# Kernel tuning notes

Hardware: AMD Instinct MI355X
Metric: run time of the kernel (lower is better)

## Reference

```python
import jax, jax.numpy as jnp
import numpy as np

NF = 10      # num RBF / Chebyshev features
GAMMA = 1.0
EMB = 10
H = 64
NHEADS = 2


def _rbf(d):
    centers = jnp.arange(1, NF + 1, dtype=d.dtype)
    return jnp.exp(-GAMMA * (centers - d[..., None]) ** 2)


def _cheb(a):
    feats = [jnp.ones_like(a), a]
    for _ in range(2, NF):
        feats.append(2 * a * feats[-1] - feats[-2])
    return jnp.stack(feats, -1)


def _gru_layer(xs, wih, whh, bih, bhh):
    # xs: [L, B, D] -> [L, B, H]; PyTorch gate order r, z, n
    B = xs.shape[1]
    def step(h, xt):
        gi = xt @ wih.T + bih
        gh = h @ whh.T + bhh
        ir, iz, inn = jnp.split(gi, 3, -1)
        hr, hz, hn = jnp.split(gh, 3, -1)
        r = jax.nn.sigmoid(ir + hr)
        z = jax.nn.sigmoid(iz + hz)
        n = jnp.tanh(inn + r * hn)
        hnew = (1 - z) * n + z * h
        return hnew, hnew
    h0 = jnp.zeros((B, H), xs.dtype)
    _, ys = jax.lax.scan(step, h0, xs)
    return ys


def _mha(x, in_w, in_b, out_w, out_b):
    B, L, E = x.shape
    hd = E // NHEADS
    qkv = x @ in_w.T + in_b
    q, k, v = jnp.split(qkv, 3, -1)
    sp = lambda t: t.reshape(B, L, NHEADS, hd).transpose(0, 2, 1, 3)
    q, k, v = sp(q), sp(k), sp(v)
    scale = 1.0 / float(np.sqrt(hd))
    att = jax.nn.softmax(jnp.einsum('bhqd,bhkd->bhqk', q, k) * scale, -1)
    o = jnp.einsum('bhqk,bhkd->bhqd', att, v).transpose(0, 2, 1, 3).reshape(B, L, E)
    return o @ out_w.T + out_b


def _ln(x, s, b):
    m = x.mean(-1, keepdims=True)
    v = ((x - m) ** 2).mean(-1, keepdims=True)
    return (x - m) / jnp.sqrt(v + 1e-5) * s + b


def setup_inputs() -> dict:
    key = jax.random.key(0)
    ks = jax.random.split(key, 48)
    N, L = 384, 256
    # bond rows: [atom_idx1, atom_idx2, bond_dist]; angle rows: [d1, d2, angle]
    idx1 = jax.random.randint(ks[0], (N, L), 1, 119).astype(jnp.float32)
    idx2 = jax.random.randint(ks[1], (N, L), 1, 119).astype(jnp.float32)
    dist = jax.random.uniform(ks[2], (N, L), minval=0.5, maxval=5.0)
    d1 = jax.random.uniform(ks[3], (N, L), minval=0.5, maxval=5.0)
    d2 = jax.random.uniform(ks[4], (N, L), minval=0.5, maxval=5.0)
    ang = jax.random.uniform(ks[5], (N, L), minval=-1.0, maxval=1.0)
    bond_x = jnp.stack([idx1, idx2, dist], 1)
    angle_x = jnp.stack([d1, d2, ang], 1)
    is_angle = (jnp.arange(N) % 3 == 2)
    x = jnp.where(is_angle[:, None, None], angle_x, bond_x)

    def nrm(k, shp, s=0.1):
        return jax.random.normal(k, shp) * s

    D_IN = 2 * EMB + NF  # 30
    inp = {
        'x': x,
        'emb': nrm(ks[6], (119, EMB), 1.0),
        'wih0': nrm(ks[7], (3 * H, D_IN)),
        'whh0': nrm(ks[8], (3 * H, H)),
        'bih0': nrm(ks[9], (3 * H,)),
        'bhh0': nrm(ks[10], (3 * H,)),
        'wih12': nrm(ks[11], (2, 3 * H, H)),
        'whh12': nrm(ks[12], (2, 3 * H, H)),
        'bih12': nrm(ks[13], (2, 3 * H)),
        'bhh12': nrm(ks[14], (2, 3 * H)),
        'in_w1': nrm(ks[15], (3 * H, H)),
        'in_b1': nrm(ks[16], (3 * H,)),
        'out_w1': nrm(ks[17], (H, H)),
        'out_b1': nrm(ks[18], (H,)),
        'in_w2': nrm(ks[19], (3 * H, H)),
        'in_b2': nrm(ks[20], (3 * H,)),
        'out_w2': nrm(ks[21], (H, H)),
        'out_b2': nrm(ks[22], (H,)),
        'ff_w1': nrm(ks[23], (1024, H)),
        'ff_b1': nrm(ks[24], (1024,)),
        'ff_w2': nrm(ks[25], (H, 1024)),
        'ff_b2': nrm(ks[26], (H,)),
        'ln1_s': jnp.ones((H,)), 'ln1_b': jnp.zeros((H,)),
        'ln2_s': jnp.ones((H,)), 'ln2_b': jnp.zeros((H,)),
        'ln3_s': jnp.ones((H,)), 'ln3_b': jnp.zeros((H,)),
        'ln4_s': jnp.ones((H,)), 'ln4_b': jnp.zeros((H,)),
        'fw1': nrm(ks[27], (256, H)), 'fb1': nrm(ks[28], (256,)),
        'fw2': nrm(ks[29], (64, 256)), 'fb2': nrm(ks[30], (64,)),
        'fw3': nrm(ks[31], (32, 64)), 'fb3': nrm(ks[32], (32,)),
        'fw4': nrm(ks[33], (1, 32)), 'fb4': nrm(ks[34], (1,)),
    }
    return inp


def reference(x, emb, wih0, whh0, bih0, bhh0, wih12, whh12, bih12, bhh12,
              in_w1, in_b1, out_w1, out_b1, in_w2, in_b2, out_w2, out_b2,
              ff_w1, ff_b1, ff_w2, ff_b2,
              ln1_s, ln1_b, ln2_s, ln2_b, ln3_s, ln3_b, ln4_s, ln4_b,
              fw1, fb1, fw2, fb2, fw3, fb3, fw4, fb4):
    # Vectorized featurization (replaces the per-triplet Python loop):
    # rows with i%3 in {0,1} are bond rows, i%3==2 are angle rows.
    i1 = jnp.clip(x[:, 0].astype(jnp.int32), 0, 118)
    i2 = jnp.clip(x[:, 1].astype(jnp.int32), 0, 118)
    bond_feat = jnp.concatenate([emb[i1], emb[i2], _rbf(x[:, 2])], -1)
    angle_feat = jnp.concatenate([_rbf(x[:, 0]), _rbf(x[:, 1]), _cheb(x[:, 2])], -1)
    is_angle = (jnp.arange(x.shape[0]) % 3 == 2)
    feat = jnp.where(is_angle[:, None, None], angle_feat, bond_feat)  # [N, L, 30]

    hs = feat.transpose(1, 0, 2)  # [L, N, 30]
    hs = _gru_layer(hs, wih0, whh0, bih0, bhh0)
    for l in range(2):
        hs = _gru_layer(hs, wih12[l], whh12[l], bih12[l], bhh12[l])
    g = hs.transpose(1, 0, 2)  # [N, L, H]

    def ffn(t):
        return jax.nn.relu(jax.nn.relu(t @ ff_w1.T + ff_b1) @ ff_w2.T + ff_b2)

    a = _mha(g, in_w1, in_b1, out_w1, out_b1)
    h = _ln(g + a, ln1_s, ln1_b)
    h = _ln(h + ffn(h), ln2_s, ln2_b)
    a = _mha(h, in_w2, in_b2, out_w2, out_b2)
    h = _ln(a + a, ln3_s, ln3_b)  # faithful to original: attn_out + attn_out
    h = _ln(h + ffn(h), ln4_s, ln4_b)
    o = h[:, -1, :]
    o = jax.nn.silu(o @ fw1.T + fb1)
    o = jax.nn.silu(o @ fw2.T + fb2)
    o = jax.nn.silu(o @ fw3.T + fb3)
    o = o @ fw4.T + fb4
    return o.squeeze(-1)
```

## Files before the change

kernel.cpp:

```cpp
#include <hip/hip_runtime.h>

static constexpr int NB   = 384;
static constexpr int SEQL = 256;
static constexpr int NROWS = NB * SEQL;

typedef short bf16x8 __attribute__((ext_vector_type(8)));
typedef float f32x4  __attribute__((ext_vector_type(4)));

union B8u {
    bf16x8 v;
    ushort us[8];
    uint4  q;
};

union F4u { float4 v; float f[4]; };

__device__ inline ushort f2bf(float f) {
    uint u = __float_as_uint(f);
    uint r = u + 0x7FFFu + ((u >> 16) & 1u);
    return (ushort)(r >> 16);
}

__device__ inline void split8(float4 a, float4 b, B8u& hi, B8u& lo) {
    float f[8] = {a.x, a.y, a.z, a.w, b.x, b.y, b.z, b.w};
    #pragma unroll
    for (int i = 0; i < 8; ++i) {
        ushort h = f2bf(f[i]);
        hi.us[i] = h;
        float fh = __uint_as_float(((uint)h) << 16);
        lo.us[i] = f2bf(f[i] - fh);
    }
}

__device__ inline float fast_rcp(float x) {
    float r = __builtin_amdgcn_rcpf(x);
    return r * (2.f - x * r);
}
__device__ inline float fast_sig(float x) {
    float e = __expf(fminf(-x, 80.f));
    return fast_rcp(1.f + e);
}
__device__ inline float fast_tanh(float a) {
    float e = __expf(fminf(2.f * fabsf(a), 80.f));
    float t = 1.f - 2.f * fast_rcp(1.f + e);
    return (a >= 0.f) ? t : -t;
}

__global__ __launch_bounds__(256) void split_kernel(
    const float* __restrict__ src, ushort* __restrict__ hi,
    ushort* __restrict__ lo, int n)
{
    int i = blockIdx.x * 256 + threadIdx.x;
    if (i < n) {
        float f = src[i];
        ushort h = f2bf(f);
        hi[i] = h;
        float fh = __uint_as_float(((uint)h) << 16);
        lo[i] = f2bf(f - fh);
    }
}

__global__ __launch_bounds__(192) void featproj_kernel(
    const float* __restrict__ x, const float* __restrict__ emb,
    const float* __restrict__ wih0, const float* __restrict__ bih0,
    float* __restrict__ X)
{
    __shared__ float F[32][33];
    const int tid = threadIdx.x;
    const int m0  = blockIdx.x * 32;

    if (tid < 96) {
        const int r   = tid & 31;
        const int grp = tid >> 5;
        const int m   = m0 + r;
        const int b   = m % NB;
        const int l   = m / NB;
        const float* xb = x + (size_t)b * (3 * SEQL);
        const float x0 = xb[l], x1 = xb[SEQL + l], x2 = xb[2 * SEQL + l];
        const bool is_angle = (b % 3) == 2;
        float o[10];
        if (is_angle) {
            if (grp < 2) {
                const float a = (grp == 0) ? x0 : x1;
                #pragma unroll
                for (int c = 0; c < 10; ++c) { float d = (float)(c + 1) - a; o[c] = __expf(-d * d); }
            } else {
                float t0 = 1.f, t1 = x2;
                o[0] = 1.f; o[1] = x2;
                #pragma unroll
                for (int c = 2; c < 10; ++c) { float t = 2.f * x2 * t1 - t0; o[c] = t; t0 = t1; t1 = t; }
            }
        } else {
            if (grp < 2) {
                const float xv = (grp == 0) ? x0 : x1;
                int idx = (int)xv; idx = idx < 0 ? 0 : (idx > 118 ? 118 : idx);
                #pragma unroll
                for (int c = 0; c < 10; ++c) o[c] = emb[idx * 10 + c];
            } else {
                #pragma unroll
                for (int c = 0; c < 10; ++c) { float d = (float)(c + 1) - x2; o[c] = __expf(-d * d); }
            }
        }
        #pragma unroll
        for (int c = 0; c < 10; ++c) F[r][grp * 10 + c] = o[c];
    }
    __syncthreads();

    float w[30];
    #pragma unroll
    for (int k = 0; k < 30; ++k) w[k] = wih0[tid * 30 + k];
    const float bj = bih0[tid];
    for (int r = 0; r < 32; ++r) {
        float acc = bj;
        #pragma unroll
        for (int k = 0; k < 30; ++k) acc += F[r][k] * w[k];
        X[(size_t)(m0 + r) * 192 + tid] = acc;
    }
}

__global__ __launch_bounds__(256, 1) void gru_mfma(
    const float* __restrict__ X, const ushort* __restrict__ WhhHi,
    const ushort* __restrict__ WhhLo, const float* __restrict__ bhh,
    float* __restrict__ Y, int out_batch_major)
{
    constexpr int PAD = 88;
    __shared__ __align__(16) ushort Hh[2][16][PAD];
    __shared__ __align__(16) ushort Hl[2][16][PAD];

    const int tid  = threadIdx.x;
    const int wt   = tid >> 6;
    const int lane = tid & 63;
    const int c    = lane & 15;
    const int g    = lane >> 4;
    const int b0   = blockIdx.x * 16;

    B8u awh[3][2], awl[3][2];
    #pragma unroll
    for (int gam = 0; gam < 3; ++gam)
        #pragma unroll
        for (int ks = 0; ks < 2; ++ks) {
            size_t off = (size_t)(64 * gam + 16 * wt + c) * 64 + 32 * ks + 8 * g;
            awh[gam][ks].q = *(const uint4*)(WhhHi + off);
            awl[gam][ks].q = *(const uint4*)(WhhLo + off);
        }
    float bg[3][4];
    #pragma unroll
    for (int gam = 0; gam < 3; ++gam)
        #pragma unroll
        for (int r = 0; r < 4; ++r)
            bg[gam][r] = bhh[64 * gam + 16 * wt + 4 * g + r];

    {
        ushort* zh = &Hh[0][0][0];
        ushort* zl = &Hl[0][0][0];
        for (int i = tid; i < 2 * 16 * PAD; i += 256) { zh[i] = 0; zl[i] = 0; }
    }
    float hold[4] = {0.f, 0.f, 0.f, 0.f};

    F4u gi[3];
    {
        const float* xp = X + ((size_t)(b0 + c)) * 192;
        #pragma unroll
        for (int gam = 0; gam < 3; ++gam)
            gi[gam].v = *(const float4*)(xp + 64 * gam + 16 * wt + 4 * g);
    }
    __syncthreads();

    for (int t = 0; t < SEQL; ++t) {
        const int p = t & 1;

        B8u bh[2], bl[2];
        #pragma unroll
        for (int ks = 0; ks < 2; ++ks) {
            const int sl = (4 * ks + g) ^ (c & 7);
            bh[ks].q = *(const uint4*)&Hh[p][c][sl * 8];
            bl[ks].q = *(const uint4*)&Hl[p][c][sl * 8];
        }

        f32x4 a0[3], a1[3];
        #pragma unroll
        for (int gam = 0; gam < 3; ++gam) {
            a0[gam] = (f32x4){bg[gam][0], bg[gam][1], bg[gam][2], bg[gam][3]};
            a1[gam] = (f32x4){0.f, 0.f, 0.f, 0.f};
        }
        #pragma unroll
        for (int gam = 0; gam < 3; ++gam) {
            a0[gam] = __builtin_amdgcn_mfma_f32_16x16x32_bf16(awh[gam][0].v, bh[0].v, a0[gam], 0, 0, 0);
            a1[gam] = __builtin_amdgcn_mfma_f32_16x16x32_bf16(awh[gam][1].v, bh[1].v, a1[gam], 0, 0, 0);
            a0[gam] = __builtin_amdgcn_mfma_f32_16x16x32_bf16(awl[gam][0].v, bh[0].v, a0[gam], 0, 0, 0);
            a1[gam] = __builtin_amdgcn_mfma_f32_16x16x32_bf16(awl[gam][1].v, bh[1].v, a1[gam], 0, 0, 0);
            a0[gam] = __builtin_amdgcn_mfma_f32_16x16x32_bf16(awh[gam][0].v, bl[0].v, a0[gam], 0, 0, 0);
            a1[gam] = __builtin_amdgcn_mfma_f32_16x16x32_bf16(awh[gam][1].v, bl[1].v, a1[gam], 0, 0, 0);
        }

        F4u ngi[3];
        {
            const int tn = (t + 1 < SEQL) ? t + 1 : t;
            const float* xp = X + ((size_t)tn * NB + b0 + c) * 192;
            #pragma unroll
            for (int gam = 0; gam < 3; ++gam)
                ngi[gam].v = *(const float4*)(xp + 64 * gam + 16 * wt + 4 * g);
        }

        float hn4[4];
        #pragma unroll
        for (int r = 0; r < 4; ++r) {
            const float gr = a0[0][r] + a1[0][r];
            const float gz = a0[1][r] + a1[1][r];
            const float gn = a0[2][r] + a1[2][r];
            const float rr = fast_sig(gi[0].f[r] + gr);
            const float zz = fast_sig(gi[1].f[r] + gz);
            const float nn = fast_tanh(gi[2].f[r] + rr * gn);
            hn4[r] = (1.f - zz) * nn + zz * hold[r];
            hold[r] = hn4[r];
        }

        {
            const size_t row = out_batch_major ? ((size_t)(b0 + c) * SEQL + t)
                                               : ((size_t)t * NB + b0 + c);
            *(float4*)&Y[row * 64 + 16 * wt + 4 * g] =
                make_float4(hn4[0], hn4[1], hn4[2], hn4[3]);
        }

        {
            ushort hh[4], hl[4];
            #pragma unroll
            for (int r = 0; r < 4; ++r) {
                ushort h = f2bf(hn4[r]);
                hh[r] = h;
                hl[r] = f2bf(hn4[r] - __uint_as_float(((uint)h) << 16));
            }
            const int sl = (2 * wt + (g >> 1)) ^ (c & 7);
            const int ad = sl * 8 + (g & 1) * 4;
            *(uint2*)&Hh[p ^ 1][c][ad] = make_uint2((uint)hh[0] | ((uint)hh[1] << 16),
                                                    (uint)hh[2] | ((uint)hh[3] << 16));
            *(uint2*)&Hl[p ^ 1][c][ad] = make_uint2((uint)hl[0] | ((uint)hl[1] << 16),
                                                    (uint)hl[2] | ((uint)hl[3] << 16));
        }
        #pragma unroll
        for (int gam = 0; gam < 3; ++gam) gi[gam].v = ngi[gam].v;

        asm volatile("s_waitcnt lgkmcnt(0)" ::: "memory");
        __builtin_amdgcn_sched_barrier(0);
        __builtin_amdgcn_s_barrier();
        __builtin_amdgcn_sched_barrier(0);
    }
}

template<int NCOLS>
__global__ __launch_bounds__(256, 2) void gemm_mfma(
    const float* __restrict__ A, const ushort* __restrict__ Whi,
    const ushort* __restrict__ Wlo, const float* __restrict__ bias,
    float* __restrict__ C)
{
    const int tid = threadIdx.x;
    const int w   = tid >> 6;
    const int lane = tid & 63;
    const int c = lane & 15;
    const int g = lane >> 4;
    const int m0 = blockIdx.x * 128 + 32 * w;

    B8u ah[2][2], al[2][2];
    #pragma unroll
    for (int rm = 0; rm < 2; ++rm) {
        const float* ap = A + (size_t)(m0 + 16 * rm + c) * 64;
        #pragma unroll
        for (int ks = 0; ks < 2; ++ks) {
            float4 v0 = *(const float4*)(ap + 32 * ks + 8 * g);
            float4 v1 = *(const float4*)(ap + 32 * ks + 8 * g + 4);
            split8(v0, v1, ah[rm][ks], al[rm][ks]);
        }
    }

    f32x4 acc[NCOLS / 16][2];
// ... 5 lines not shown
            acc[nt][rm] = (f32x4){bv, bv, bv, bv};
    }

    #pragma unroll
    for (int nt = 0; nt < NCOLS / 16; ++nt) {
        B8u wh[2], wl[2];
        #pragma unroll
        for (int ks = 0; ks < 2; ++ks) {
            size_t off = (size_t)(16 * nt + c) * 64 + 32 * ks + 8 * g;
            wh[ks].q = *(const uint4*)(Whi + off);
            wl[ks].q = *(const uint4*)(Wlo + off);
        }
        #pragma unroll
        for (int rm = 0; rm < 2; ++rm)
            #pragma unroll
            for (int ks = 0; ks < 2; ++ks) {
                acc[nt][rm] = __builtin_amdgcn_mfma_f32_16x16x32_bf16(ah[rm][ks].v, wh[ks].v, acc[nt][rm], 0, 0, 0);
                acc[nt][rm] = __builtin_amdgcn_mfma_f32_16x16x32_bf16(al[rm][ks].v, wh[ks].v, acc[nt][rm], 0, 0, 0);
                acc[nt][rm] = __builtin_amdgcn_mfma_f32_16x16x32_bf16(ah[rm][ks].v, wl[ks].v, acc[nt][rm], 0, 0, 0);
            }
    }

    #pragma unroll
    for (int nt = 0; nt < NCOLS / 16; ++nt)
        #pragma unroll
        for (int rm = 0; rm < 2; ++rm)
            #pragma unroll
            for (int reg = 0; reg < 4; ++reg) {
                int row = m0 + 16 * rm + 4 * g + reg;
                C[(size_t)row * NCOLS + 16 * nt + c] = acc[nt][rm][reg];
            }
}

__global__ __launch_bounds__(256, 2) void ffn_mfma(
    const float* __restrict__ Xin,
    const ushort* __restrict__ W1hi, const ushort* __restrict__ W1lo,
    const ushort* __restrict__ W2hi, const ushort* __restrict__ W2lo,
    const float* __restrict__ b1, const float* __restrict__ b2,
    float* __restrict__ Out)
{
    __shared__ __align__(16) ushort sW1h[64 * 72], sW1l[64 * 72];
    __shared__ __align__(16) ushort sW2h[64 * 72], sW2l[64 * 72];
    __shared__ __align__(16) ushort sHh[128 * 72], sHl[128 * 72];
    __shared__ float sb1[64];

    const int tid = threadIdx.x;
    const int w   = tid >> 6;
    const int lane = tid & 63;
    const int c = lane & 15;
    const int g = lane >> 4;
    const int r0 = blockIdx.x * 128;

    B8u xh[2][2], xl[2][2];
    #pragma unroll
    for (int rm = 0; rm < 2; ++rm) {
        const float* ap = Xin + (size_t)(r0 + 32 * w + 16 * rm + c) * 64;
        #pragma unroll
        for (int ks = 0; ks < 2; ++ks) {
            float4 v0 = *(const float4*)(ap + 32 * ks + 8 * g);
            float4 v1 = *(const float4*)(ap + 32 * ks + 8 * g + 4);
            split8(v0, v1, xh[rm][ks], xl[rm][ks]);
        }
    }

    f32x4 acc2[4][2];
    #pragma unroll
    for (int jt = 0; jt < 4; ++jt) {
        float bv = b2[16 * jt + c];
        #pragma unroll
        for (int mt = 0; mt < 2; ++mt)
            acc2[jt][mt] = (f32x4){bv, bv, bv, bv};
// ... 65 lines not shown
                                               (uint)hh[2] | ((uint)hh[3] << 16));
                *(uint2*)&sHl[el] = make_uint2((uint)hl[0] | ((uint)hl[1] << 16),
                                               (uint)hl[2] | ((uint)hl[3] << 16));
            }
        asm volatile("s_waitcnt lgkmcnt(0)" ::: "memory");
        __builtin_amdgcn_sched_barrier(0);

        #pragma unroll
        for (int ks = 0; ks < 2; ++ks) {
            B8u ahh[2], ahl[2], bwh[4], bwl[4];
            #pragma unroll
            for (int mt = 0; mt < 2; ++mt) {
                int el = (32 * w + 16 * mt + c) * 72 + 32 * ks + 8 * g;
                ahh[mt].q = *(const uint4*)&sHh[el];
                ahl[mt].q = *(const uint4*)&sHl[el];
            }
            #pragma unroll
            for (int jt = 0; jt < 4; ++jt) {
                int el = (16 * jt + c) * 72 + 32 * ks + 8 * g;
                bwh[jt].q = *(const uint4*)&sW2h[el];
                bwl[jt].q = *(const uint4*)&sW2l[el];
            }
            #pragma unroll
            for (int jt = 0; jt < 4; ++jt)
                #pragma unroll
                for (int mt = 0; mt < 2; ++mt) {
                    acc2[jt][mt] = __builtin_amdgcn_mfma_f32_16x16x32_bf16(ahh[mt].v, bwh[jt].v, acc2[jt][mt], 0, 0, 0);
                    acc2[jt][mt] = __builtin_amdgcn_mfma_f32_16x16x32_bf16(ahl[mt].v, bwh[jt].v, acc2[jt][mt], 0, 0, 0);
                    acc2[jt][mt] = __builtin_amdgcn_mfma_f32_16x16x32_bf16(ahh[mt].v, bwl[jt].v, acc2[jt][mt], 0, 0, 0);
                }
        }
    }

    #pragma unroll
    for (int jt = 0; jt < 4; ++jt)
        #pragma unroll
        for (int mt = 0; mt < 2; ++mt)
            #pragma unroll
            for (int reg = 0; reg < 4; ++reg) {
                int row = r0 + 32 * w + 16 * mt + 4 * g + reg;
                Out[(size_t)row * 64 + 16 * jt + c] = fmaxf(acc2[jt][mt][reg], 0.f);
            }
}

__global__ __launch_bounds__(256, 2) void attn_mfma(
    const float* __restrict__ QKV, float* __restrict__ Out)
{
    __shared__ __align__(16) ushort Ph[4][4096];
    __shared__ __align__(16) ushort Pl[4][4096];

    const int h = blockIdx.x;
    const int b = blockIdx.y;
    const int tid = threadIdx.x;
    const int w = tid >> 6;
    const int lane = tid & 63;
    const int c = lane & 15;
    const int g = lane >> 4;
    const float scale = 0.17677669529663687f;

    const float* base = QKV + (size_t)b * SEQL * 192;
    ushort* phw = Ph[w];
    ushort* plw = Pl[w];

    B8u qh[4], ql[4];
    #pragma unroll
    for (int qt = 0; qt < 4; ++qt) {
        const float* p = base + (size_t)(64 * w + 16 * qt + c) * 192 + h * 32 + 8 * g;
        float4 v0 = *(const float4*)p;
        float4 v1 = *(const float4*)(p + 4);
        v0.x *= scale; v0.y *= scale; v0.z *= scale; v0.w *= scale;
        v1.x *= scale; v1.y *= scale; v1.z *= scale; v1.w *= scale;
        split8(v0, v1, qh[qt], ql[qt]);
    }

    f32x4 o[2][4];
// ... 83 lines not shown

        asm volatile("s_waitcnt lgkmcnt(0)" ::: "memory");
        __builtin_amdgcn_sched_barrier(0);

        #pragma unroll
        for (int ks = 0; ks < 2; ++ks)
            #pragma unroll
            for (int qt = 0; qt < 4; ++qt) {
                const int ql_ = 16 * qt + c;
                const int orr = (ks * 4 + g) ^ (ql_ & 7);
                const int addr = ql_ * 64 + orr * 8;
                B8u pbh, pbl;
                pbh.q = *(const uint4*)&phw[addr];
                pbl.q = *(const uint4*)&plw[addr];
                #pragma unroll
                for (int dt = 0; dt < 2; ++dt) {
                    o[dt][qt] = __builtin_amdgcn_mfma_f32_16x16x32_bf16(vh[ks][dt].v, pbh.v, o[dt][qt], 0, 0, 0);
                    o[dt][qt] = __builtin_amdgcn_mfma_f32_16x16x32_bf16(vl[ks][dt].v, pbh.v, o[dt][qt], 0, 0, 0);
                    o[dt][qt] = __builtin_amdgcn_mfma_f32_16x16x32_bf16(vh[ks][dt].v, pbl.v, o[dt][qt], 0, 0, 0);
                }
            }
    }

    #pragma unroll
    for (int qt = 0; qt < 4; ++qt) {
        const float inv = 1.f / lrun[qt];
        const size_t row = (size_t)b * SEQL + 64 * w + 16 * qt + c;
        #pragma unroll
        for (int dt = 0; dt < 2; ++dt)
            #pragma unroll
            for (int r = 0; r < 4; ++r)
                Out[row * 64 + h * 32 + 16 * dt + 4 * g + r] = o[dt][qt][r] * inv;
    }
}

__global__ __launch_bounds__(256) void add_ln_kernel(
    const float* __restrict__ A, const float* __restrict__ B,
    const float* __restrict__ s, const float* __restrict__ bb,
    float* __restrict__ O)
{
    const size_t row = (size_t)blockIdx.x * 4 + (threadIdx.x >> 6);
    const int lane = threadIdx.x & 63;
    float v = A[row * 64 + lane] + B[row * 64 + lane];
    float sum = v;
    #pragma unroll
    for (int off = 32; off; off >>= 1) sum += __shfl_xor(sum, off);
    const float mean = sum * (1.f / 64.f);
    const float d = v - mean;
    float sq = d * d;
    #pragma unroll
    for (int off = 32; off; off >>= 1) sq += __shfl_xor(sq, off);
    const float var = sq * (1.f / 64.f);
    O[row * 64 + lane] = d * rsqrtf(var + 1e-5f) * s[lane] + bb[lane];
}

__global__ __launch_bounds__(256) void head_kernel(
    const float* __restrict__ Hf,
    const float* __restrict__ fw1, const float* __restrict__ fb1,
    const float* __restrict__ fw2, const float* __restrict__ fb2,
    const float* __restrict__ fw3, const float* __restrict__ fb3,
    const float* __restrict__ fw4, const float* __restrict__ fb4,
    float* __restrict__ out)
{
    const int b = blockIdx.x;
    const int tid = threadIdx.x;
    __shared__ float t0[64], t1[256], t2[64], t3[32];
    if (tid < 64) t0[tid] = Hf[((size_t)b * SEQL + (SEQL - 1)) * 64 + tid];
    __syncthreads();
    {
        float acc = fb1[tid];
        #pragma unroll 4
        for (int k = 0; k < 64; ++k) acc += t0[k] * fw1[tid * 64 + k];
        t1[tid] = acc / (1.f + __expf(-acc));
    }
    __syncthreads();
    if (tid < 64) {
        float acc = fb2[tid];
        #pragma unroll 4
        for (int k = 0; k < 256; ++k) acc += t1[k] * fw2[tid * 256 + k];
        t2[tid] = acc / (1.f + __expf(-acc));
    }
    __syncthreads();
    if (tid < 32) {
        float acc = fb3[tid];
        #pragma unroll 4
        for (int k = 0; k < 64; ++k) acc += t2[k] * fw3[tid * 64 + k];
// ... 46 lines not shown
    const float* fw2   = (const float*)d_in[32];
    const float* fb2   = (const float*)d_in[33];
    const float* fw3   = (const float*)d_in[34];
    const float* fb3   = (const float*)d_in[35];
    const float* fw4   = (const float*)d_in[36];
    const float* fb4   = (const float*)d_in[37];

    float* ws = (float*)d_ws;
    float* X  = ws;
    float* S0 = X  + (size_t)NROWS * 192;
    float* S1 = S0 + (size_t)NROWS * 64;
    float* S2 = S1 + (size_t)NROWS * 64;

    ushort* bf = (ushort*)(S2 + (size_t)NROWS * 64);
    ushort* ffw1hi = bf;
    ushort* ffw1lo = ffw1hi + 65536;
    ushort* ffw2hi = ffw1lo + 65536;
    ushort* ffw2lo = ffw2hi + 65536;
    ushort* wghi   = ffw2lo + 65536;
    ushort* wglo   = wghi + 24576;
    ushort* q1hi   = wglo + 24576;
    ushort* q1lo   = q1hi + 12288;
    ushort* q2hi   = q1lo + 12288;
    ushort* q2lo   = q2hi + 12288;
    ushort* o1hi   = q2lo + 12288;
    ushort* o1lo   = o1hi + 4096;
    ushort* o2hi   = o1lo + 4096;
    ushort* o2lo   = o2hi + 4096;
    ushort* w0hi   = o2lo + 4096;
    ushort* w0lo   = w0hi + 12288;
    ushort* w12hi  = w0lo + 12288;
    ushort* w12lo  = w12hi + 24576;

    split_kernel<<<65536 / 256, 256, 0, stream>>>(ff_w1, ffw1hi, ffw1lo, 65536);
    split_kernel<<<65536 / 256, 256, 0, stream>>>(ff_w2, ffw2hi, ffw2lo, 65536);
    split_kernel<<<24576 / 256, 256, 0, stream>>>(wih12, wghi, wglo, 24576);
    split_kernel<<<12288 / 256, 256, 0, stream>>>(in_w1, q1hi, q1lo, 12288);
    split_kernel<<<12288 / 256, 256, 0, stream>>>(in_w2, q2hi, q2lo, 12288);
    split_kernel<<<4096 / 256, 256, 0, stream>>>(out_w1, o1hi, o1lo, 4096);
    split_kernel<<<4096 / 256, 256, 0, stream>>>(out_w2, o2hi, o2lo, 4096);
    split_kernel<<<12288 / 256, 256, 0, stream>>>(whh0, w0hi, w0lo, 12288);
    split_kernel<<<24576 / 256, 256, 0, stream>>>(whh12, w12hi, w12lo, 24576);

    featproj_kernel<<<NROWS / 32, 192, 0, stream>>>(x, emb, wih0, bih0, X);
    gru_mfma<<<NB / 16, 256, 0, stream>>>(X, w0hi, w0lo, bhh0, S0, 0);
    gemm_mfma<192><<<NROWS / 128, 256, 0, stream>>>(S0, wghi, wglo, bih12, X);
    gru_mfma<<<NB / 16, 256, 0, stream>>>(X, w12hi, w12lo, bhh12, S1, 0);
    gemm_mfma<192><<<NROWS / 128, 256, 0, stream>>>(S1, wghi + 12288, wglo + 12288, bih12 + 192, X);
    gru_mfma<<<NB / 16, 256, 0, stream>>>(X, w12hi + 12288, w12lo + 12288, bhh12 + 192, S0, 1);

    gemm_mfma<192><<<NROWS / 128, 256, 0, stream>>>(S0, q1hi, q1lo, in_b1, X);
    attn_mfma<<<dim3(2, NB), 256, 0, stream>>>(X, S1);
    gemm_mfma<64><<<NROWS / 128, 256, 0, stream>>>(S1, o1hi, o1lo, out_b1, S2);
    add_ln_kernel<<<NROWS / 4, 256, 0, stream>>>(S0, S2, ln1_s, ln1_b, S1);
    ffn_mfma<<<NROWS / 128, 256, 0, stream>>>(S1, ffw1hi, ffw1lo, ffw2hi, ffw2lo, ff_b1, ff_b2, S2);
    add_ln_kernel<<<NROWS / 4, 256, 0, stream>>>(S1, S2, ln2_s, ln2_b, S0);

    gemm_mfma<192><<<NROWS / 128, 256, 0, stream>>>(S0, q2hi, q2lo, in_b2, X);
    attn_mfma<<<dim3(2, NB), 256, 0, stream>>>(X, S1);
    gemm_mfma<64><<<NROWS / 128, 256, 0, stream>>>(S1, o2hi, o2lo, out_b2, S2);
    add_ln_kernel<<<NROWS / 4, 256, 0, stream>>>(S2, S2, ln3_s, ln3_b, S1);
    ffn_mfma<<<NROWS / 128, 256, 0, stream>>>(S1, ffw1hi, ffw1lo, ffw2hi, ffw2lo, ff_b1, ff_b2, S2);
    add_ln_kernel<<<NROWS / 4, 256, 0, stream>>>(S1, S2, ln4_s, ln4_b, S0);

    head_kernel<<<NB, 256, 0, stream>>>(S0, fw1, fb1, fw2, fb2, fw3, fb3, fw4, fb4,
                                        (float*)d_out);
    (void)in_sizes; (void)n_in; (void)out_size; (void)ws_size;
}
```

Before: 1.120 ms.

## Fuse three GRU layers into one wavefront-pipelined kernel with in-kernel input projections

Replaces three sequential GRU launches and two input-projection GEMMs with a single 768-thread kernel in which each group of 4 waves runs one layer. The layers are skewed by one timestep and pass hidden states through shared memory. Layers 1 and 2 compute their input projection with extra MFMAs on the previous layer's shared-memory state, so the intermediate sequences never round-trip through global memory. This removes two serial 256-step recurrences from the critical path and cuts HBM traffic, but each step now does more MFMA work and the block needs more registers per thread.

```diff
diff --git a/kernel.cpp b/kernel.cpp
--- a/kernel.cpp
+++ b/kernel.cpp
@@ -118,128 +118,179 @@
     }
 }
 
-__global__ __launch_bounds__(256, 1) void gru_mfma(
-    const float* __restrict__ X, const ushort* __restrict__ WhhHi,
-    const ushort* __restrict__ WhhLo, const float* __restrict__ bhh,
-    float* __restrict__ Y, int out_batch_major)
+__global__ __launch_bounds__(768) void gru3_mfma(
+    const float* __restrict__ X,
+    const ushort* __restrict__ W0hi,  const ushort* __restrict__ W0lo,
+    const ushort* __restrict__ W12hi, const ushort* __restrict__ W12lo,
+    const ushort* __restrict__ WIhi,  const ushort* __restrict__ WIlo,
+    const float* __restrict__ bhh0,  const float* __restrict__ bhh12,
+    const float* __restrict__ bih12, float* __restrict__ Y)
 {
     constexpr int PAD = 88;
-    __shared__ __align__(16) ushort Hh[2][16][PAD];
-    __shared__ __align__(16) ushort Hl[2][16][PAD];
-
-    const int tid  = threadIdx.x;
-    const int wt   = tid >> 6;
-    const int lane = tid & 63;
-    const int c    = lane & 15;
-    const int g    = lane >> 4;
-    const int b0   = blockIdx.x * 16;
-
-    B8u awh[3][2], awl[3][2];
+    __shared__ __align__(16) ushort Hh[3][2][16][PAD];
+    __shared__ __align__(16) ushort Hl[3][2][16][PAD];
+
+    const int tid   = threadIdx.x;
+    const int stage = tid >> 8;
+    const int wt    = (tid >> 6) & 3;
+    const int lane  = tid & 63;
+    const int c     = lane & 15;
+    const int g     = lane >> 4;
+    const int b0    = blockIdx.x * 16;
+
+    const ushort* rh_src = (stage == 0) ? W0hi : (W12hi + (size_t)(stage - 1) * 12288);
+    const ushort* rl_src = (stage == 0) ? W0lo : (W12lo + (size_t)(stage - 1) * 12288);
+    B8u rwh[3][2], rwl[3][2];
     #pragma unroll
     for (int gam = 0; gam < 3; ++gam)
         #pragma unroll
         for (int ks = 0; ks < 2; ++ks) {
             size_t off = (size_t)(64 * gam + 16 * wt + c) * 64 + 32 * ks + 8 * g;
-            awh[gam][ks].q = *(const uint4*)(WhhHi + off);
-            awl[gam][ks].q = *(const uint4*)(WhhLo + off);
-        }
-    float bg[3][4];
-    #pragma unroll
-    for (int gam = 0; gam < 3; ++gam)
-        #pragma unroll
-        for (int r = 0; r < 4; ++r)
-            bg[gam][r] = bhh[64 * gam + 16 * wt + 4 * g + r];
+            rwh[gam][ks].q = *(const uint4*)(rh_src + off);
+            rwl[gam][ks].q = *(const uint4*)(rl_src + off);
+        }
+    B8u pwh[3][2], pwl[3][2];
+    if (stage > 0) {
+        const ushort* ph_src = WIhi + (size_t)(stage - 1) * 12288;
+        const ushort* pl_src = WIlo + (size_t)(stage - 1) * 12288;
+        #pragma unroll
+        for (int gam = 0; gam < 3; ++gam)
+            #pragma unroll
+            for (int ks = 0; ks < 2; ++ks) {
+                size_t off = (size_t)(64 * gam + 16 * wt + c) * 64 + 32 * ks + 8 * g;
+                pwh[gam][ks].q = *(const uint4*)(ph_src + off);
+                pwl[gam][ks].q = *(const uint4*)(pl_src + off);
+            }
+    }
+
+    const float* bhp = (stage == 0) ? bhh0 : (bhh12 + (stage - 1) * 192);
+    const float* bip = bih12 + (stage > 0 ? (stage - 1) * 192 : 0);
+    float brz[2][4], bnh_[4], bni_[4];
+    #pragma unroll
+    for (int r = 0; r < 4; ++r) {
+        const int j = 16 * wt + 4 * g + r;
+        brz[0][r] = bhp[j]      + (stage > 0 ? bip[j]      : 0.f);
+        brz[1][r] = bhp[64 + j] + (stage > 0 ? bip[64 + j] : 0.f);
+        bnh_[r]   = bhp[128 + j];
+        bni_[r]   = (stage > 0) ? bip[128 + j] : 0.f;
+    }
 
     {
-        ushort* zh = &Hh[0][0][0];
-        ushort* zl = &Hl[0][0][0];
-        for (int i = tid; i < 2 * 16 * PAD; i += 256) { zh[i] = 0; zl[i] = 0; }
+        ushort* zh = &Hh[0][0][0][0];
+        ushort* zl = &Hl[0][0][0][0];
+        for (int i = tid; i < 3 * 2 * 16 * PAD; i += 768) { zh[i] = 0; zl[i] = 0; }
     }
     float hold[4] = {0.f, 0.f, 0.f, 0.f};
 
     F4u gi[3];
-    {
-        const float* xp = X + ((size_t)(b0 + c)) * 192;
+    if (stage == 0) {
+        const float* xp = X + (size_t)(b0 + c) * 192;
         #pragma unroll
         for (int gam = 0; gam < 3; ++gam)
             gi[gam].v = *(const float4*)(xp + 64 * gam + 16 * wt + 4 * g);
     }
     __syncthreads();
 
-    for (int t = 0; t < SEQL; ++t) {
-        const int p = t & 1;
-
-        B8u bh[2], bl[2];
-        #pragma unroll
-        for (int ks = 0; ks < 2; ++ks) {
-            const int sl = (4 * ks + g) ^ (c & 7);
-            bh[ks].q = *(const uint4*)&Hh[p][c][sl * 8];
-            bl[ks].q = *(const uint4*)&Hl[p][c][sl * 8];
-        }
-
-        f32x4 a0[3], a1[3];
-        #pragma unroll
-        for (int gam = 0; gam < 3; ++gam) {
-            a0[gam] = (f32x4){bg[gam][0], bg[gam][1], bg[gam][2], bg[gam][3]};
-            a1[gam] = (f32x4){0.f, 0.f, 0.f, 0.f};
-        }
-        #pragma unroll
-        for (int gam = 0; gam < 3; ++gam) {
-            a0[gam] = __builtin_amdgcn_mfma_f32_16x16x32_bf16(awh[gam][0].v, bh[0].v, a0[gam], 0, 0, 0);
-            a1[gam] = __builtin_amdgcn_mfma_f32_16x16x32_bf16(awh[gam][1].v, bh[1].v, a1[gam], 0, 0, 0);
-            a0[gam] = __builtin_amdgcn_mfma_f32_16x16x32_bf16(awl[gam][0].v, bh[0].v, a0[gam], 0, 0, 0);
-            a1[gam] = __builtin_amdgcn_mfma_f32_16x16x32_bf16(awl[gam][1].v, bh[1].v, a1[gam], 0, 0, 0);
-            a0[gam] = __builtin_amdgcn_mfma_f32_16x16x32_bf16(awh[gam][0].v, bl[0].v, a0[gam], 0, 0, 0);
-            a1[gam] = __builtin_amdgcn_mfma_f32_16x16x32_bf16(awh[gam][1].v, bl[1].v, a1[gam], 0, 0, 0);
-        }
-
-        F4u ngi[3];
-        {
-            const int tn = (t + 1 < SEQL) ? t + 1 : t;
-            const float* xp = X + ((size_t)tn * NB + b0 + c) * 192;
-            #pragma unroll
-            for (int gam = 0; gam < 3; ++gam)
-                ngi[gam].v = *(const float4*)(xp + 64 * gam + 16 * wt + 4 * g);
-        }
-
-        float hn4[4];
-        #pragma unroll
-        for (int r = 0; r < 4; ++r) {
-            const float gr = a0[0][r] + a1[0][r];
-            const float gz = a0[1][r] + a1[1][r];
-            const float gn = a0[2][r] + a1[2][r];
-            const float rr = fast_sig(gi[0].f[r] + gr);
-            const float zz = fast_sig(gi[1].f[r] + gz);
-            const float nn = fast_tanh(gi[2].f[r] + rr * gn);
-            hn4[r] = (1.f - zz) * nn + zz * hold[r];
-            hold[r] = hn4[r];
-        }
-
-        {
-            const size_t row = out_batch_major ? ((size_t)(b0 + c) * SEQL + t)
-                                               : ((size_t)t * NB + b0 + c);
-            *(float4*)&Y[row * 64 + 16 * wt + 4 * g] =
-                make_float4(hn4[0], hn4[1], hn4[2], hn4[3]);
-        }
-
-        {
-            ushort hh[4], hl[4];
+    #pragma unroll 1
+    for (int s = 0; s < SEQL + 2; ++s) {
+        const int t = s - stage;
+        const int p = s & 1;
+        if (t >= 0 && t < SEQL) {
+            f32x4 aR  = (f32x4){brz[0][0], brz[0][1], brz[0][2], brz[0][3]};
+            f32x4 aZ  = (f32x4){brz[1][0], brz[1][1], brz[1][2], brz[1][3]};
+            f32x4 aNh = (f32x4){bnh_[0], bnh_[1], bnh_[2], bnh_[3]};
+            f32x4 aNi = (f32x4){bni_[0], bni_[1], bni_[2], bni_[3]};
+
+            if (stage > 0) {
+                B8u bhp2[2], blp2[2];
+                #pragma unroll
+                for (int ks = 0; ks < 2; ++ks) {
+                    const int sl = (4 * ks + g) ^ (c & 7);
+                    bhp2[ks].q = *(const uint4*)&Hh[stage - 1][p ^ 1][c][sl * 8];
+                    blp2[ks].q = *(const uint4*)&Hl[stage - 1][p ^ 1][c][sl * 8];
+                }
+                #pragma unroll
+                for (int ks = 0; ks < 2; ++ks) {
+                    aR  = __builtin_amdgcn_mfma_f32_16x16x32_bf16(pwh[0][ks].v, bhp2[ks].v, aR, 0, 0, 0);
+                    aR  = __builtin_amdgcn_mfma_f32_16x16x32_bf16(pwl[0][ks].v, bhp2[ks].v, aR, 0, 0, 0);
+                    aR  = __builtin_amdgcn_mfma_f32_16x16x32_bf16(pwh[0][ks].v, blp2[ks].v, aR, 0, 0, 0);
+                    aZ  = __builtin_amdgcn_mfma_f32_16x16x32_bf16(pwh[1][ks].v, bhp2[ks].v, aZ, 0, 0, 0);
+                    aZ  = __builtin_amdgcn_mfma_f32_16x16x32_bf16(pwl[1][ks].v, bhp2[ks].v, aZ, 0, 0, 0);
+                    aZ  = __builtin_amdgcn_mfma_f32_16x16x32_bf16(pwh[1][ks].v, blp2[ks].v, aZ, 0, 0, 0);
+                    aNi = __builtin_amdgcn_mfma_f32_16x16x32_bf16(pwh[2][ks].v, bhp2[ks].v, aNi, 0, 0, 0);
+                    aNi = __builtin_amdgcn_mfma_f32_16x16x32_bf16(pwl[2][ks].v, bhp2[ks].v, aNi, 0, 0, 0);
+                    aNi = __builtin_amdgcn_mfma_f32_16x16x32_bf16(pwh[2][ks].v, blp2[ks].v, aNi, 0, 0, 0);
+                }
+            }
+            {
+                B8u bhr[2], blr[2];
+                #pragma unroll
+                for (int ks = 0; ks < 2; ++ks) {
+                    const int sl = (4 * ks + g) ^ (c & 7);
+                    bhr[ks].q = *(const uint4*)&Hh[stage][p ^ 1][c][sl * 8];
+                    blr[ks].q = *(const uint4*)&Hl[stage][p ^ 1][c][sl * 8];
+                }
+                #pragma unroll
+                for (int ks = 0; ks < 2; ++ks) {
+                    aR  = __builtin_amdgcn_mfma_f32_16x16x32_bf16(rwh[0][ks].v, bhr[ks].v, aR, 0, 0, 0);
+                    aR  = __builtin_amdgcn_mfma_f32_16x16x32_bf16(rwl[0][ks].v, bhr[ks].v, aR, 0, 0, 0);
+                    aR  = __builtin_amdgcn_mfma_f32_16x16x32_bf16(rwh[0][ks].v, blr[ks].v, aR, 0, 0, 0);
+                    aZ  = __builtin_amdgcn_mfma_f32_16x16x32_bf16(rwh[1][ks].v, bhr[ks].v, aZ, 0, 0, 0);
+                    aZ  = __builtin_amdgcn_mfma_f32_16x16x32_bf16(rwl[1][ks].v, bhr[ks].v, aZ, 0, 0, 0);
+                    aZ  = __builtin_amdgcn_mfma_f32_16x16x32_bf16(rwh[1][ks].v, blr[ks].v, aZ, 0, 0, 0);
+                    aNh = __builtin_amdgcn_mfma_f32_16x16x32_bf16(rwh[2][ks].v, bhr[ks].v, aNh, 0, 0, 0);
+                    aNh = __builtin_amdgcn_mfma_f32_16x16x32_bf16(rwl[2][ks].v, bhr[ks].v, aNh, 0, 0, 0);
+                    aNh = __builtin_amdgcn_mfma_f32_16x16x32_bf16(rwh[2][ks].v, blr[ks].v, aNh, 0, 0, 0);
+                }
+            }
+
+            F4u ngi[3];
+            if (stage == 0) {
+                const int tn = (t + 1 < SEQL) ? t + 1 : t;
+                const float* xp = X + ((size_t)tn * NB + b0 + c) * 192;
+                #pragma unroll
+                for (int gam = 0; gam < 3; ++gam)
+                    ngi[gam].v = *(const float4*)(xp + 64 * gam + 16 * wt + 4 * g);
+            }
+
+            float hn4[4];
             #pragma unroll
             for (int r = 0; r < 4; ++r) {
-                ushort h = f2bf(hn4[r]);
-                hh[r] = h;
-                hl[r] = f2bf(hn4[r] - __uint_as_float(((uint)h) << 16));
-            }
-            const int sl = (2 * wt + (g >> 1)) ^ (c & 7);
-            const int ad = sl * 8 + (g & 1) * 4;
-            *(uint2*)&Hh[p ^ 1][c][ad] = make_uint2((uint)hh[0] | ((uint)hh[1] << 16),
-                                                    (uint)hh[2] | ((uint)hh[3] << 16));
-            *(uint2*)&Hl[p ^ 1][c][ad] = make_uint2((uint)hl[0] | ((uint)hl[1] << 16),
-                                                    (uint)hl[2] | ((uint)hl[3] << 16));
-        }
-        #pragma unroll
-        for (int gam = 0; gam < 3; ++gam) gi[gam].v = ngi[gam].v;
-
+                const float xr = (stage == 0) ? gi[0].f[r] : 0.f;
+                const float xz = (stage == 0) ? gi[1].f[r] : 0.f;
+                const float xn = (stage == 0) ? gi[2].f[r] : aNi[r];
+                const float rr = fast_sig(xr + aR[r]);
+                const float zz = fast_sig(xz + aZ[r]);
+                const float nn = fast_tanh(xn + rr * aNh[r]);
+                hn4[r] = (1.f - zz) * nn + zz * hold[r];
+                hold[r] = hn4[r];
+            }
+
+            {
+                ushort hh[4], hl[4];
+                #pragma unroll
+                for (int r = 0; r < 4; ++r) {
+                    ushort h = f2bf(hn4[r]);
+                    hh[r] = h;
+                    hl[r] = f2bf(hn4[r] - __uint_as_float(((uint)h) << 16));
+                }
+                const int sl = (2 * wt + (g >> 1)) ^ (c & 7);
+                const int ad = sl * 8 + (g & 1) * 4;
+                *(uint2*)&Hh[stage][p][c][ad] = make_uint2((uint)hh[0] | ((uint)hh[1] << 16),
+                                                           (uint)hh[2] | ((uint)hh[3] << 16));
+                *(uint2*)&Hl[stage][p][c][ad] = make_uint2((uint)hl[0] | ((uint)hl[1] << 16),
+                                                           (uint)hl[2] | ((uint)hl[3] << 16));
+            }
+            if (stage == 2) {
+                const size_t row = (size_t)(b0 + c) * SEQL + t;
+                *(float4*)&Y[row * 64 + 16 * wt + 4 * g] =
+                    make_float4(hn4[0], hn4[1], hn4[2], hn4[3]);
+            }
+            if (stage == 0) {
+                #pragma unroll
+                for (int gam = 0; gam < 3; ++gam) gi[gam].v = ngi[gam].v;
+            }
+        }
         asm volatile("s_waitcnt lgkmcnt(0)" ::: "memory");
         __builtin_amdgcn_sched_barrier(0);
         __builtin_amdgcn_s_barrier();
@@ -748,11 +799,8 @@
     split_kernel<<<24576 / 256, 256, 0, stream>>>(whh12, w12hi, w12lo, 24576);
 
     featproj_kernel<<<NROWS / 32, 192, 0, stream>>>(x, emb, wih0, bih0, X);
-    gru_mfma<<<NB / 16, 256, 0, stream>>>(X, w0hi, w0lo, bhh0, S0, 0);
-    gemm_mfma<192><<<NROWS / 128, 256, 0, stream>>>(S0, wghi, wglo, bih12, X);
-    gru_mfma<<<NB / 16, 256, 0, stream>>>(X, w12hi, w12lo, bhh12, S1, 0);
-    gemm_mfma<192><<<NROWS / 128, 256, 0, stream>>>(S1, wghi + 12288, wglo + 12288, bih12 + 192, X);
-    gru_mfma<<<NB / 16, 256, 0, stream>>>(X, w12hi + 12288, w12lo + 12288, bhh12 + 192, S0, 1);
+    gru3_mfma<<<NB / 16, 768, 0, stream>>>(X, w0hi, w0lo, w12hi, w12lo,
+                                           wghi, wglo, bhh0, bhh12, bih12, S0);
 
     gemm_mfma<192><<<NROWS / 128, 256, 0, stream>>>(S0, q1hi, q1lo, in_b1, X);
     attn_mfma<<<dim3(2, NB), 256, 0, stream>>>(X, S1);
```

Result: slower. 1.169 ms (+4.4%).

## Fuse residual-add LayerNorm into out-projection and FFN epilogues; batch weight splits

Applied to the files above, without the earlier changes.

Removes the four standalone add+LayerNorm kernels. The residual add and LayerNorm now run in the epilogues of a new out-projection GEMM kernel and of the FFN kernel, with cross-lane shuffle reductions over the 16 column lanes. The nine per-weight bf16 hi/lo split launches are merged into one multi-segment kernel. This saves launches and several full-activation global round trips. In exchange, variance is computed as E[x²]−mean², which is slightly less numerically stable, and epilogue register pressure rises.

```diff
diff --git a/kernel.cpp b/kernel.cpp
--- a/kernel.cpp
+++ b/kernel.cpp
@@ -46,18 +46,34 @@
     return (a >= 0.f) ? t : -t;
 }
 
-__global__ __launch_bounds__(256) void split_kernel(
-    const float* __restrict__ src, ushort* __restrict__ hi,
-    ushort* __restrict__ lo, int n)
+__device__ inline void split1(const float* s, ushort* h, ushort* l, int i) {
+    float f = s[i];
+    ushort hh = f2bf(f);
+    h[i] = hh;
+    l[i] = f2bf(f - __uint_as_float(((uint)hh) << 16));
+}
+
+__global__ __launch_bounds__(256) void split_all(
+    const float* s0, const float* s1, const float* s2, const float* s3,
+    const float* s4, const float* s5, const float* s6, const float* s7,
+    const float* s8,
+    ushort* h0, ushort* h1, ushort* h2, ushort* h3, ushort* h4,
+    ushort* h5, ushort* h6, ushort* h7, ushort* h8,
+    ushort* l0, ushort* l1, ushort* l2, ushort* l3, ushort* l4,
+    ushort* l5, ushort* l6, ushort* l7, ushort* l8)
 {
-    int i = blockIdx.x * 256 + threadIdx.x;
-    if (i < n) {
-        float f = src[i];
-        ushort h = f2bf(f);
-        hi[i] = h;
-        float fh = __uint_as_float(((uint)h) << 16);
-        lo[i] = f2bf(f - fh);
-    }
+    const int b = blockIdx.x;
+    const float* s; ushort* h; ushort* l; int base;
+    if      (b < 256) { s = s0; h = h0; l = l0; base = 0; }
+    else if (b < 512) { s = s1; h = h1; l = l1; base = 256; }
+    else if (b < 608) { s = s2; h = h2; l = l2; base = 512; }
+    else if (b < 656) { s = s3; h = h3; l = l3; base = 608; }
+    else if (b < 704) { s = s4; h = h4; l = l4; base = 656; }
+    else if (b < 720) { s = s5; h = h5; l = l5; base = 704; }
+    else if (b < 736) { s = s6; h = h6; l = l6; base = 720; }
+    else if (b < 784) { s = s7; h = h7; l = l7; base = 736; }
+    else              { s = s8; h = h8; l = l8; base = 784; }
+    split1(s, h, l, (b - base) * 256 + threadIdx.x);
 }
 
 __global__ __launch_bounds__(192) void featproj_kernel(
@@ -311,11 +327,106 @@
             }
 }
 
-__global__ __launch_bounds__(256, 2) void ffn_mfma(
+__global__ __launch_bounds__(256, 2) void gemm_ln_mfma(
+    const float* __restrict__ A, const ushort* __restrict__ Whi,
+    const ushort* __restrict__ Wlo, const float* __restrict__ bias,
+    const float* __restrict__ resid,
+    const float* __restrict__ lns, const float* __restrict__ lnb,
+    float* __restrict__ O)
+{
+    const int tid = threadIdx.x;
+    const int w   = tid >> 6;
+    const int lane = tid & 63;
+    const int c = lane & 15;
+    const int g = lane >> 4;
+    const int m0 = blockIdx.x * 128 + 32 * w;
+
+    B8u ah[2][2], al[2][2];
+    #pragma unroll
+    for (int rm = 0; rm < 2; ++rm) {
+        const float* ap = A + (size_t)(m0 + 16 * rm + c) * 64;
+        #pragma unroll
+        for (int ks = 0; ks < 2; ++ks) {
+            float4 v0 = *(const float4*)(ap + 32 * ks + 8 * g);
+            float4 v1 = *(const float4*)(ap + 32 * ks + 8 * g + 4);
+            split8(v0, v1, ah[rm][ks], al[rm][ks]);
+        }
+    }
+
+    f32x4 acc[4][2];
+    #pragma unroll
+    for (int nt = 0; nt < 4; ++nt) {
+        float bv = bias[16 * nt + c];
+        #pragma unroll
+        for (int rm = 0; rm < 2; ++rm)
+            acc[nt][rm] = (f32x4){bv, bv, bv, bv};
+    }
+
+    #pragma unroll
+    for (int nt = 0; nt < 4; ++nt) {
+        B8u wh[2], wl[2];
+        #pragma unroll
+        for (int ks = 0; ks < 2; ++ks) {
+            size_t off = (size_t)(16 * nt + c) * 64 + 32 * ks + 8 * g;
+            wh[ks].q = *(const uint4*)(Whi + off);
+            wl[ks].q = *(const uint4*)(Wlo + off);
+        }
+        #pragma unroll
+        for (int rm = 0; rm < 2; ++rm)
+            #pragma unroll
+            for (int ks = 0; ks < 2; ++ks) {
+                acc[nt][rm] = __builtin_amdgcn_mfma_f32_16x16x32_bf16(ah[rm][ks].v, wh[ks].v, acc[nt][rm], 0, 0, 0);
+                acc[nt][rm] = __builtin_amdgcn_mfma_f32_16x16x32_bf16(al[rm][ks].v, wh[ks].v, acc[nt][rm], 0, 0, 0);
+                acc[nt][rm] = __builtin_amdgcn_mfma_f32_16x16x32_bf16(ah[rm][ks].v, wl[ks].v, acc[nt][rm], 0, 0, 0);
+            }
+    }
+
+    float vv[4][2][4];
+    #pragma unroll
+    for (int nt = 0; nt < 4; ++nt)
+        #pragma unroll
+        for (int rm = 0; rm < 2; ++rm)
+            #pragma unroll
+            for (int reg = 0; reg < 4; ++reg) {
+                const int row = m0 + 16 * rm + 4 * g + reg;
+                const float a = acc[nt][rm][reg];
+                const float r_ = resid ? resid[(size_t)row * 64 + 16 * nt + c] : a;
+                vv[nt][rm][reg] = a + r_;
+            }
+
+    float sv[4], bv[4];
+    #pragma unroll
+    for (int nt = 0; nt < 4; ++nt) { sv[nt] = lns[16 * nt + c]; bv[nt] = lnb[16 * nt + c]; }
+
+    #pragma unroll
+    for (int rm = 0; rm < 2; ++rm)
+        #pragma unroll
+        for (int reg = 0; reg < 4; ++reg) {
+            float sum = vv[0][rm][reg] + vv[1][rm][reg] + vv[2][rm][reg] + vv[3][rm][reg];
+            float sq  = vv[0][rm][reg]*vv[0][rm][reg] + vv[1][rm][reg]*vv[1][rm][reg]
+                      + vv[2][rm][reg]*vv[2][rm][reg] + vv[3][rm][reg]*vv[3][rm][reg];
+            #pragma unroll
+            for (int off = 1; off < 16; off <<= 1) {
+                sum += __shfl_xor(sum, off);
+                sq  += __shfl_xor(sq,  off);
+            }
+            const float mean = sum * (1.f / 64.f);
+            const float var  = sq * (1.f / 64.f) - mean * mean;
+            const float inv  = rsqrtf(var + 1e-5f);
+            const int row = m0 + 16 * rm + 4 * g + reg;
+            #pragma unroll
+            for (int nt = 0; nt < 4; ++nt)
+                O[(size_t)row * 64 + 16 * nt + c] =
+                    (vv[nt][rm][reg] - mean) * inv * sv[nt] + bv[nt];
+        }
+}
+
+__global__ __launch_bounds__(256, 2) void ffn_ln_mfma(
     const float* __restrict__ Xin,
     const ushort* __restrict__ W1hi, const ushort* __restrict__ W1lo,
     const ushort* __restrict__ W2hi, const ushort* __restrict__ W2lo,
     const float* __restrict__ b1, const float* __restrict__ b2,
+    const float* __restrict__ lns, const float* __restrict__ lnb,
     float* __restrict__ Out)
 {
     __shared__ __align__(16) ushort sW1h[64 * 72], sW1l[64 * 72];
@@ -447,15 +558,43 @@
         }
     }
 
+    float vv[4][2][4];
     #pragma unroll
     for (int jt = 0; jt < 4; ++jt)
         #pragma unroll
         for (int mt = 0; mt < 2; ++mt)
             #pragma unroll
             for (int reg = 0; reg < 4; ++reg) {
-                int row = r0 + 32 * w + 16 * mt + 4 * g + reg;
-                Out[(size_t)row * 64 + 16 * jt + c] = fmaxf(acc2[jt][mt][reg], 0.f);
-            }
+                const int row = r0 + 32 * w + 16 * mt + 4 * g + reg;
+                vv[jt][mt][reg] = fmaxf(acc2[jt][mt][reg], 0.f) +
+                                  Xin[(size_t)row * 64 + 16 * jt + c];
+            }
+
+    float sv[4], bv[4];
+    #pragma unroll
+    for (int jt = 0; jt < 4; ++jt) { sv[jt] = lns[16 * jt + c]; bv[jt] = lnb[16 * jt + c]; }
+
+    #pragma unroll
+    for (int mt = 0; mt < 2; ++mt)
+        #pragma unroll
+        for (int reg = 0; reg < 4; ++reg) {
+            float sum = vv[0][mt][reg] + vv[1][mt][reg] + vv[2][mt][reg] + vv[3][mt][reg];
+            float sq  = vv[0][mt][reg]*vv[0][mt][reg] + vv[1][mt][reg]*vv[1][mt][reg]
+                      + vv[2][mt][reg]*vv[2][mt][reg] + vv[3][mt][reg]*vv[3][mt][reg];
+            #pragma unroll
+            for (int off = 1; off < 16; off <<= 1) {
+                sum += __shfl_xor(sum, off);
+                sq  += __shfl_xor(sq,  off);
+            }
+            const float mean = sum * (1.f / 64.f);
+            const float var  = sq * (1.f / 64.f) - mean * mean;
+            const float inv  = rsqrtf(var + 1e-5f);
+            const int row = r0 + 32 * w + 16 * mt + 4 * g + reg;
+            #pragma unroll
+            for (int jt = 0; jt < 4; ++jt)
+                Out[(size_t)row * 64 + 16 * jt + c] =
+                    (vv[jt][mt][reg] - mean) * inv * sv[jt] + bv[jt];
+        }
 }
 
 __global__ __launch_bounds__(256, 2) void attn_mfma(
@@ -605,26 +744,6 @@
             for (int r = 0; r < 4; ++r)
                 Out[row * 64 + h * 32 + 16 * dt + 4 * g + r] = o[dt][qt][r] * inv;
     }
-}
-
-__global__ __launch_bounds__(256) void add_ln_kernel(
-    const float* __restrict__ A, const float* __restrict__ B,
-    const float* __restrict__ s, const float* __restrict__ bb,
-    float* __restrict__ O)
-{
-    const size_t row = (size_t)blockIdx.x * 4 + (threadIdx.x >> 6);
-    const int lane = threadIdx.x & 63;
-    float v = A[row * 64 + lane] + B[row * 64 + lane];
-    float sum = v;
-    #pragma unroll
-    for (int off = 32; off; off >>= 1) sum += __shfl_xor(sum, off);
-    const float mean = sum * (1.f / 64.f);
-    const float d = v - mean;
-    float sq = d * d;
-    #pragma unroll
-    for (int off = 32; off; off >>= 1) sq += __shfl_xor(sq, off);
-    const float var = sq * (1.f / 64.f);
-    O[row * 64 + lane] = d * rsqrtf(var + 1e-5f) * s[lane] + bb[lane];
 }
 
 __global__ __launch_bounds__(256) void head_kernel(
@@ -737,15 +856,10 @@
     ushort* w12hi  = w0lo + 12288;
     ushort* w12lo  = w12hi + 24576;
 
-    split_kernel<<<65536 / 256, 256, 0, stream>>>(ff_w1, ffw1hi, ffw1lo, 65536);
-    split_kernel<<<65536 / 256, 256, 0, stream>>>(ff_w2, ffw2hi, ffw2lo, 65536);
-    split_kernel<<<24576 / 256, 256, 0, stream>>>(wih12, wghi, wglo, 24576);
-    split_kernel<<<12288 / 256, 256, 0, stream>>>(in_w1, q1hi, q1lo, 12288);
-    split_kernel<<<12288 / 256, 256, 0, stream>>>(in_w2, q2hi, q2lo, 12288);
-    split_kernel<<<4096 / 256, 256, 0, stream>>>(out_w1, o1hi, o1lo, 4096);
-    split_kernel<<<4096 / 256, 256, 0, stream>>>(out_w2, o2hi, o2lo, 4096);
-    split_kernel<<<12288 / 256, 256, 0, stream>>>(whh0, w0hi, w0lo, 12288);
-    split_kernel<<<24576 / 256, 256, 0, stream>>>(whh12, w12hi, w12lo, 24576);
+    split_all<<<880, 256, 0, stream>>>(
+        ff_w1, ff_w2, wih12, in_w1, in_w2, out_w1, out_w2, whh0, whh12,
+        ffw1hi, ffw2hi, wghi, q1hi, q2hi, o1hi, o2hi, w0hi, w12hi,
+        ffw1lo, ffw2lo, wglo, q1lo, q2lo, o1lo, o2lo, w0lo, w12lo);
 
     featproj_kernel<<<NROWS / 32, 192, 0, stream>>>(x, emb, wih0, bih0, X);
     gru_mfma<<<NB / 16, 256, 0, stream>>>(X, w0hi, w0lo, bhh0, S0, 0);
@@ -756,19 +870,19 @@
 
     gemm_mfma<192><<<NROWS / 128, 256, 0, stream>>>(S0, q1hi, q1lo, in_b1, X);
     attn_mfma<<<dim3(2, NB), 256, 0, stream>>>(X, S1);
-    gemm_mfma<64><<<NROWS / 128, 256, 0, stream>>>(S1, o1hi, o1lo, out_b1, S2);
-    add_ln_kernel<<<NROWS / 4, 256, 0, stream>>>(S0, S2, ln1_s, ln1_b, S1);
-    ffn_mfma<<<NROWS / 128, 256, 0, stream>>>(S1, ffw1hi, ffw1lo, ffw2hi, ffw2lo, ff_b1, ff_b2, S2);
-    add_ln_kernel<<<NROWS / 4, 256, 0, stream>>>(S1, S2, ln2_s, ln2_b, S0);
+    gemm_ln_mfma<<<NROWS / 128, 256, 0, stream>>>(S1, o1hi, o1lo, out_b1,
+                                                  S0, ln1_s, ln1_b, S2);
+    ffn_ln_mfma<<<NROWS / 128, 256, 0, stream>>>(S2, ffw1hi, ffw1lo, ffw2hi, ffw2lo,
+                                                 ff_b1, ff_b2, ln2_s, ln2_b, S0);
 
     gemm_mfma<192><<<NROWS / 128, 256, 0, stream>>>(S0, q2hi, q2lo, in_b2, X);
     attn_mfma<<<dim3(2, NB), 256, 0, stream>>>(X, S1);
-    gemm_mfma<64><<<NROWS / 128, 256, 0, stream>>>(S1, o2hi, o2lo, out_b2, S2);
-    add_ln_kernel<<<NROWS / 4, 256, 0, stream>>>(S2, S2, ln3_s, ln3_b, S1);
-    ffn_mfma<<<NROWS / 128, 256, 0, stream>>>(S1, ffw1hi, ffw1lo, ffw2hi, ffw2lo, ff_b1, ff_b2, S2);
-    add_ln_kernel<<<NROWS / 4, 256, 0, stream>>>(S1, S2, ln4_s, ln4_b, S0);
-
-    head_kernel<<<NB, 256, 0, stream>>>(S0, fw1, fb1, fw2, fb2, fw3, fb3, fw4, fb4,
+    gemm_ln_mfma<<<NROWS / 128, 256, 0, stream>>>(S1, o2hi, o2lo, out_b2,
+                                                  nullptr, ln3_s, ln3_b, S2);
+    ffn_ln_mfma<<<NROWS / 128, 256, 0, stream>>>(S2, ffw1hi, ffw1lo, ffw2hi, ffw2lo,
+                                                 ff_b1, ff_b2, ln4_s, ln4_b, S1);
+
+    head_kernel<<<NB, 256, 0, stream>>>(S1, fw1, fb1, fw2, fb2, fw3, fb3, fw4, fb4,
                                         (float*)d_out);
     (void)in_sizes; (void)n_in; (void)out_size; (void)ws_size;
 }
```

Result: faster. 1.055 ms (-5.8%).
